# Kernel tuning notes

Measured on AMD Instinct MI355X. Metric: run time of the kernel, lower is better.

The kernel has to match this reference:

```python
import jax, jax.numpy as jnp
import numpy as np

C, CP, H, D, N, B = 128, 16, 8, 16, 2048, 1
INF = 1e8


def _ln(x, w=None, b=None, eps=1e-5):
    mu = jnp.mean(x, axis=-1, keepdims=True)
    var = jnp.var(x, axis=-1, keepdims=True)
    y = (x - mu) * jax.lax.rsqrt(var + eps)
    if w is not None:
        y = y * w
    if b is not None:
        y = y + b
    return y


def _ada_ln(a, s, sln_w, gw, gb, skw):
    # AdaLN: non-affine LN on a, weight-only LN on s, sigmoid gate + skip from s
    a = _ln(a)
    s = _ln(s, sln_w)
    return jax.nn.sigmoid(s @ gw + gb) * a + s @ skw


def _betas(n, n_keys=128, inf=INF):
    # centers at 16 + 32k; query row i belongs to window i//32, keys within +/- n_keys//2 of center
    i = jnp.arange(n)
    c = 16 + 32 * (i // 32)
    j = jnp.arange(n)
    ok = (j[None, :] >= (c - n_keys // 2)[:, None]) & (j[None, :] < (c + n_keys // 2)[:, None])
    return jnp.where(ok, 0.0, -inf).astype(jnp.float32)


def _forward(atom_single, atom_proj, atom_pair, mask,
             a_sln_w, a_gate_w, a_gate_b, a_skip_w,
             wq, bq, wk, wv, wg, bg, wo, bo,
             lnz_w, lnz_b, wz, wog, bog,
             t_sln_w, t_gate_w, t_gate_b, t_skip_w,
             w_sw, w_hid, w_out, t_wog, t_bog):
    bs, n, _ = atom_single.shape
    betas = _betas(n)
    # ---- AttentionPairBias (input_gating=True, residual handled outside) ----
    a = _ada_ln(atom_single, atom_proj, a_sln_w, a_gate_w, a_gate_b, a_skip_w)
    q = (a @ wq + bq).reshape(bs, n, H, D)
    k = (a @ wk).reshape(bs, n, H, D)
    v = (a @ wv).reshape(bs, n, H, D)
    pair_bias = _ln(atom_pair, lnz_w, lnz_b) @ wz            # (bs, n, n, H)
    pair_bias = jnp.transpose(pair_bias, (0, 3, 1, 2)) + betas  # (bs, H, n, n)
    mask_bias = (INF * (mask - 1.0))[:, None, None, :]          # (bs, 1, 1, n)
    logits = jnp.einsum('bqhd,bkhd->bhqk', q, k) / np.float32(np.sqrt(D))
    logits = logits + pair_bias + mask_bias
    probs = jax.nn.softmax(logits, axis=-1)
    o = jnp.einsum('bhqk,bkhd->bqhd', probs, v)
    g = jax.nn.sigmoid(a @ wg + bg).reshape(bs, n, H, D)
    o = (o * g).reshape(bs, n, H * D) @ wo + bo
    o = jax.nn.sigmoid(atom_proj @ wog + bog) * o             # conditioned output gate
    atom_single = atom_single + o
    # ---- ConditionedTransitionBlock (SwiGLU, n=2) ----
    t = _ada_ln(atom_single, atom_proj, t_sln_w, t_gate_w, t_gate_b, t_skip_w)
    hidden = jax.nn.silu(t @ w_sw) * (t @ w_hid)              # (bs, n, 2C)
    t_out = jax.nn.sigmoid(atom_proj @ t_wog + t_bog) * (hidden @ w_out)
    return atom_single + t_out


def setup_inputs() -> dict:
    key = jax.random.key(0)
    ks = iter(jax.random.split(key, 40))
    rn = lambda shape, s=1.0: jax.random.normal(next(ks), shape, jnp.float32) * s
    p = 0.05
    return {
        "atom_single": rn((B, N, C)),
        "atom_proj": rn((B, N, C)),
        "atom_pair": rn((B, N, N, CP)),
        "mask": jnp.ones((B, N), jnp.float32),
        "a_sln_w": jnp.ones((C,), jnp.float32), "a_gate_w": rn((C, C), p), "a_gate_b": jnp.zeros((C,), jnp.float32), "a_skip_w": rn((C, C), p),
        "wq": rn((C, C), p), "bq": jnp.zeros((C,), jnp.float32),
        "wk": rn((C, C), p), "wv": rn((C, C), p),
        "wg": rn((C, C), p), "bg": jnp.ones((C,), jnp.float32),
        "wo": rn((C, C), p), "bo": jnp.zeros((C,), jnp.float32),
        "lnz_w": jnp.ones((CP,), jnp.float32), "lnz_b": jnp.zeros((CP,), jnp.float32), "wz": rn((CP, H), p),
        "wog": rn((C, C), p), "bog": jnp.full((C,), -2.0, jnp.float32),
        "t_sln_w": jnp.ones((C,), jnp.float32), "t_gate_w": rn((C, C), p), "t_gate_b": jnp.zeros((C,), jnp.float32), "t_skip_w": rn((C, C), p),
        "w_sw": rn((C, 2 * C), p), "w_hid": rn((C, 2 * C), p), "w_out": rn((2 * C, C), p),
        "t_wog": rn((C, C), p), "t_bog": jnp.full((C,), -2.0, jnp.float32),
    }


def reference(atom_single, atom_proj, atom_pair, mask,
              a_sln_w, a_gate_w, a_gate_b, a_skip_w,
              wq, bq, wk, wv, wg, bg, wo, bo,
              lnz_w, lnz_b, wz, wog, bog,
              t_sln_w, t_gate_w, t_gate_b, t_skip_w,
              w_sw, w_hid, w_out, t_wog, t_bog):
    out = _forward(atom_single, atom_proj, atom_pair, mask,
                   a_sln_w, a_gate_w, a_gate_b, a_skip_w,
                   wq, bq, wk, wv, wg, bg, wo, bo,
                   lnz_w, lnz_b, wz, wog, bog,
                   t_sln_w, t_gate_w, t_gate_b, t_skip_w,
                   w_sw, w_hid, w_out, t_wog, t_bog)
    return (out, atom_proj, atom_pair)
```

## Files before the change

### kernel.cpp

```cpp
#include <hip/hip_runtime.h>
#include <math.h>

#define NN 2048
#define CC 128
#define HH 8
#define DD 16
#define NKEY 128
#define INFV 1e8f
#define NPR ((long)NN * CC / 4)
#define NCPTOT (NPR + (long)NN * NN * 4)
#define SLOT 2176
#define ANP 36
#define ASLOT 1152

__device__ __forceinline__ float sigm(float x) { return 1.f / (1.f + expf(-x)); }

struct Args {
  const float *atom_single, *atom_proj, *atom_pair, *mask;
  const float *a_sln_w, *a_gate_w, *a_gate_b, *a_skip_w;
  const float *wq, *bq, *wk, *wv, *wg, *bg, *wo, *bo;
  const float *lnz_w, *lnz_b, *wz, *wog, *bog;
  const float *t_sln_w, *t_gate_w, *t_gate_b, *t_skip_w;
  const float *w_sw, *w_hid, *w_out, *t_wog, *t_bog;
  float *out;
  float *s_ln_t, *a_mat, *qm, *km, *vm, *gm, *ogm, *single2, *t_mat, *hidden, *bias;
  long cut[8];
};

__device__ __forceinline__ void copy_span(const Args& a, int s, long rb, long nb, int tid) {
  long c0 = a.cut[s], c1 = a.cut[s + 1];
  const float4* proj4 = (const float4*)a.atom_proj;
  const float4* pair4 = (const float4*)a.atom_pair;
  float4* dst = (float4*)(a.out + (long)NN * CC);
  long stride = nb * 256;
  long i = c0 + rb * 256 + tid;
  for (; i + 3 * stride < c1; i += 4 * stride) {
    long i1 = i + stride, i2 = i + 2 * stride, i3 = i + 3 * stride;
    float4 x0 = (i  < NPR) ? proj4[i]  : pair4[i  - NPR];
    float4 x1 = (i1 < NPR) ? proj4[i1] : pair4[i1 - NPR];
    float4 x2 = (i2 < NPR) ? proj4[i2] : pair4[i2 - NPR];
    float4 x3 = (i3 < NPR) ? proj4[i3] : pair4[i3 - NPR];
    dst[i] = x0; dst[i1] = x1; dst[i2] = x2; dst[i3] = x3;
  }
  for (; i < c1; i += stride) dst[i] = (i < NPR) ? proj4[i] : pair4[i - NPR];
}

__device__ __forceinline__ void gsingle_pf(float* sm, int tid,
    const float* __restrict__ A1, const float* __restrict__ B1, int lda1, int ldb1, int K1,
    int r0, int c0, float acc1[4][4]) {
  float* buf0 = sm;
  float* buf1 = sm + 2 * SLOT;
  int tr = (tid >> 4) * 4, tc = (tid & 15) * 4;
  int ar = tid >> 5, ak = tid & 31;
  int bk = tid >> 6, bc = tid & 63;
  float pA[2][8], pB[2][8];
  auto LD = [&](int kb, int s) {
#pragma unroll
    for (int j = 0; j < 8; ++j) {
      pA[s][j] = A1[(long)(r0 + ar + 8 * j) * lda1 + kb + ak];
      pB[s][j] = B1[(long)(kb + bk + 4 * j) * ldb1 + c0 + bc];
    }
  };
  auto WR = [&](float* buf, int s) {
    float* B1s_ = buf + SLOT;
#pragma unroll
    for (int j = 0; j < 8; ++j) {
      buf[ak * 68 + ar + 8 * j] = pA[s][j];
      B1s_[(bk + 4 * j) * 68 + bc] = pB[s][j];
    }
  };
  auto CMP = [&](float* cur) {
    float* As_ = cur;
    float* B1s_ = cur + SLOT;
#pragma unroll 4
    for (int k = 0; k < 32; ++k) {
      float4 a1 = *(const float4*)&As_[k * 68 + tr];
      float4 b1 = *(const float4*)&B1s_[k * 68 + tc];
      float a1v[4] = {a1.x, a1.y, a1.z, a1.w};
      float b1v[4] = {b1.x, b1.y, b1.z, b1.w};
#pragma unroll
      for (int i = 0; i < 4; ++i)
#pragma unroll
        for (int j = 0; j < 4; ++j) acc1[i][j] = fmaf(a1v[i], b1v[j], acc1[i][j]);
    }
  };
  int nk = K1 / 32;
  LD(0, 0);
  if (nk > 1) LD(32, 1);
  WR(buf0, 0);
  __syncthreads();
  for (int kt = 0; kt < nk; kt += 2) {
    if (kt + 2 < nk) LD((kt + 2) * 32, 0);
    if (kt + 1 < nk) WR(buf1, 1);
    CMP(buf0);
    __syncthreads();
    if (kt + 1 >= nk) break;
    if (kt + 3 < nk) LD((kt + 3) * 32, 1);
    if (kt + 2 < nk) WR(buf0, 0);
    CMP(buf1);
    __syncthreads();
  }
}

template <bool SHA>
__device__ __forceinline__ void gdual32(float* sm, int tid,
    const float* __restrict__ A1, const float* __restrict__ B1, int lda1, int ldb1, int K1,
    const float* __restrict__ A2, const float* __restrict__ B2, int lda2, int ldb2, int K2,
    int r0, int c0, float acc1[2][4], float acc2[2][4]) {
  const int offB1 = ASLOT;
  const int offA2 = ASLOT + SLOT;
  const int offB2 = SHA ? (ASLOT + SLOT) : (2 * ASLOT + SLOT);
  const int bufsz = SHA ? (ASLOT + 2 * SLOT) : (2 * ASLOT + 2 * SLOT);
  float* buf0 = sm;
  float* buf1 = sm + bufsz;
  int tr2 = (tid >> 4) * 2, tc4 = (tid & 15) * 4;
  int ar = tid & 31, ak4 = (tid >> 5) * 4;
  int bk = tid >> 6, bc = tid & 63;
  float4 vA1[2], vA2[2];
  float pB1[2][8], pB2[2][8];

  auto LD = [&](int kb, int s, bool twof) {
    vA1[s] = *(const float4*)&A1[(long)(r0 + ar) * lda1 + kb + ak4];
#pragma unroll
    for (int j = 0; j < 8; ++j)
      pB1[s][j] = B1[(long)(kb + bk + 4 * j) * ldb1 + c0 + bc];
    if (twof) {
      if constexpr (!SHA) vA2[s] = *(const float4*)&A2[(long)(r0 + ar) * lda2 + kb + ak4];
#pragma unroll
      for (int j = 0; j < 8; ++j)
        pB2[s][j] = B2[(long)(kb + bk + 4 * j) * ldb2 + c0 + bc];
    }
  };
  auto WR = [&](float* buf, int s, bool twof) {
    float* As_ = buf;
    float* B1s_ = buf + offB1;
    As_[(ak4 + 0) * ANP + ar] = vA1[s].x;
    As_[(ak4 + 1) * ANP + ar] = vA1[s].y;
    As_[(ak4 + 2) * ANP + ar] = vA1[s].z;
    As_[(ak4 + 3) * ANP + ar] = vA1[s].w;
#pragma unroll
    for (int j = 0; j < 8; ++j) B1s_[(bk + 4 * j) * 68 + bc] = pB1[s][j];
    if (twof) {
      float* B2s_ = buf + offB2;
      if constexpr (!SHA) {
        float* A2s_ = buf + offA2;
        A2s_[(ak4 + 0) * ANP + ar] = vA2[s].x;
        A2s_[(ak4 + 1) * ANP + ar] = vA2[s].y;
        A2s_[(ak4 + 2) * ANP + ar] = vA2[s].z;
        A2s_[(ak4 + 3) * ANP + ar] = vA2[s].w;
      }
#pragma unroll
      for (int j = 0; j < 8; ++j) B2s_[(bk + 4 * j) * 68 + bc] = pB2[s][j];
    }
  };
  auto CMP = [&](float* cur, bool twoc) {
    float* As_ = cur;
    float* B1s_ = cur + offB1;
    float* A2s_ = cur + offA2;
    float* B2s_ = cur + offB2;
    if (twoc) {
#pragma unroll 4
      for (int k = 0; k < 32; ++k) {
        float2 a1 = *(const float2*)&As_[k * ANP + tr2];
        float4 b1 = *(const float4*)&B1s_[k * 68 + tc4];
        float4 b2 = *(const float4*)&B2s_[k * 68 + tc4];
        float2 a2;
        if constexpr (SHA) a2 = a1; else a2 = *(const float2*)&A2s_[k * ANP + tr2];
        float a1v[2] = {a1.x, a1.y};
        float a2v[2] = {a2.x, a2.y};
        float b1v[4] = {b1.x, b1.y, b1.z, b1.w};
        float b2v[4] = {b2.x, b2.y, b2.z, b2.w};
#pragma unroll
        for (int i = 0; i < 2; ++i)
#pragma unroll
          for (int j = 0; j < 4; ++j) {
            acc1[i][j] = fmaf(a1v[i], b1v[j], acc1[i][j]);
            acc2[i][j] = fmaf(a2v[i], b2v[j], acc2[i][j]);
          }
      }
    } else {
#pragma unroll 4
      for (int k = 0; k < 32; ++k) {
        float2 a1 = *(const float2*)&As_[k * ANP + tr2];
        float4 b1 = *(const float4*)&B1s_[k * 68 + tc4];
        float a1v[2] = {a1.x, a1.y};
        float b1v[4] = {b1.x, b1.y, b1.z, b1.w};
#pragma unroll
        for (int i = 0; i < 2; ++i)
#pragma unroll
          for (int j = 0; j < 4; ++j) acc1[i][j] = fmaf(a1v[i], b1v[j], acc1[i][j]);
      }
    }
  };

  int nk = K1 / 32;
  LD(0, 0, 0 < K2);
  if (nk > 1) LD(32, 1, 32 < K2);
  WR(buf0, 0, 0 < K2);
  __syncthreads();
  for (int kt = 0; kt < nk; kt += 2) {
    if (kt + 2 < nk) LD((kt + 2) * 32, 0, (kt + 2) * 32 < K2);
    if (kt + 1 < nk) WR(buf1, 1, (kt + 1) * 32 < K2);
    CMP(buf0, kt * 32 < K2);
    __syncthreads();
    if (kt + 1 >= nk) break;
    if (kt + 3 < nk) LD((kt + 3) * 32, 1, (kt + 3) * 32 < K2);
    if (kt + 2 < nk) WR(buf0, 0, (kt + 2) * 32 < K2);
    CMP(buf1, (kt + 1) * 32 < K2);
    __syncthreads();
  }
}

__device__ __forceinline__ void gdual32_ln(float* sm, int tid,
    const float* __restrict__ proj, const float* __restrict__ w_ln,
    const float* __restrict__ B1, const float* __restrict__ B2,
    int r0, int c0, const float* sst, float acc1[2][4], float acc2[2][4]) {
  const int offB1 = ASLOT;
  const int offB2 = ASLOT + SLOT;
  const int bufsz = ASLOT + 2 * SLOT;
  float* buf0 = sm;
  float* buf1 = sm + bufsz;
  int tr2 = (tid >> 4) * 2, tc4 = (tid & 15) * 4;
  int ar = tid & 31, ak4 = (tid >> 5) * 4;
  int bk = tid >> 6, bc = tid & 63;
  float4 vA1[2];
  float pB1[2][8], pB2[2][8];

  auto LD = [&](int kb, int s) {
    float4 raw = *(const float4*)&proj[(long)(r0 + ar) * CC + kb + ak4];
    float4 wv = *(const float4*)&w_ln[kb + ak4];
    float mu = sst[2 * ar], rs = sst[2 * ar + 1];
    vA1[s].x = (raw.x - mu) * rs * wv.x;
    vA1[s].y = (raw.y - mu) * rs * wv.y;
    vA1[s].z = (raw.z - mu) * rs * wv.z;
    vA1[s].w = (raw.w - mu) * rs * wv.w;
#pragma unroll
    for (int j = 0; j < 8; ++j) {
      pB1[s][j] = B1[(long)(kb + bk + 4 * j) * CC + c0 + bc];
      pB2[s][j] = B2[(long)(kb + bk + 4 * j) * CC + c0 + bc];
    }
  };
  auto WR = [&](float* buf, int s) {
    float* B1s_ = buf + offB1;
    float* B2s_ = buf + offB2;
    buf[(ak4 + 0) * ANP + ar] = vA1[s].x;
    buf[(ak4 + 1) * ANP + ar] = vA1[s].y;
    buf[(ak4 + 2) * ANP + ar] = vA1[s].z;
    buf[(ak4 + 3) * ANP + ar] = vA1[s].w;
#pragma unroll
    for (int j = 0; j < 8; ++j) {
      B1s_[(bk + 4 * j) * 68 + bc] = pB1[s][j];
      B2s_[(bk + 4 * j) * 68 + bc] = pB2[s][j];
    }
  };
  auto CMP = [&](float* cur) {
    float* As_ = cur;
    float* B1s_ = cur + offB1;
    float* B2s_ = cur + offB2;
#pragma unroll 4
    for (int k = 0; k < 32; ++k) {
      float2 a1 = *(const float2*)&As_[k * ANP + tr2];
      float4 b1 = *(const float4*)&B1s_[k * 68 + tc4];
      float4 b2 = *(const float4*)&B2s_[k * 68 + tc4];
      float a1v[2] = {a1.x, a1.y};
      float b1v[4] = {b1.x, b1.y, b1.z, b1.w};
      float b2v[4] = {b2.x, b2.y, b2.z, b2.w};
#pragma unroll
      for (int i = 0; i < 2; ++i)
#pragma unroll
        for (int j = 0; j < 4; ++j) {
          acc1[i][j] = fmaf(a1v[i], b1v[j], acc1[i][j]);
          acc2[i][j] = fmaf(a1v[i], b2v[j], acc2[i][j]);
        }
    }
  };

  LD(0, 0);
  LD(32, 1);
  WR(buf0, 0);
  __syncthreads();
  LD(64, 0);
  WR(buf1, 1);
  CMP(buf0);
  __syncthreads();
  LD(96, 1);
  WR(buf0, 0);
  CMP(buf1);
  __syncthreads();
  WR(buf1, 1);
  CMP(buf0);
  __syncthreads();
  CMP(buf1);
  __syncthreads();
}

__device__ __forceinline__ void bias_stage(const Args& a, long lo, long hi,
                                           int bid, int nb, int tid, float* sm) {
  float* swz = sm;
  float* swn = sm + 128;
  float* sbn = sm + 144;
  if (tid < 128) swz[tid] = a.wz[tid];
  else if (tid < 144) swn[tid - 128] = a.lnz_w[tid - 128];
  else if (tid < 160) sbn[tid - 144] = a.lnz_b[tid - 144];
  __syncthreads();
  for (long e = lo + bid * 256 + tid; e < hi; e += (long)nb * 256) {
    int q = (int)(e >> 7), kk = (int)(e & 127);
    int k = (q >> 5) * 32 - 48 + kk;
    float o[HH];
    if (k >= 0 && k < NN) {
      const float4* p = (const float4*)(a.atom_pair + ((long)q * NN + k) * 16);
      float4 x0 = p[0], x1 = p[1], x2 = p[2], x3 = p[3];
      float x[16] = {x0.x, x0.y, x0.z, x0.w, x1.x, x1.y, x1.z, x1.w,
                     x2.x, x2.y, x2.z, x2.w, x3.x, x3.y, x3.z, x3.w};
      float s = 0.f, ss = 0.f;
#pragma unroll
      for (int c = 0; c < 16; ++c) { s += x[c]; ss += x[c] * x[c]; }
      float mu = s * (1.f / 16.f);
      float r = rsqrtf(ss * (1.f / 16.f) - mu * mu + 1e-5f);
#pragma unroll
      for (int h = 0; h < HH; ++h) o[h] = 0.f;
#pragma unroll
      for (int c = 0; c < 16; ++c) {
        float y = (x[c] - mu) * r * swn[c] + sbn[c];
#pragma unroll
        for (int h = 0; h < HH; ++h) o[h] = fmaf(y, swz[c * HH + h], o[h]);
      }
      float mb = INFV * (a.mask[k] - 1.f);
#pragma unroll
      for (int h = 0; h < HH; ++h) o[h] += mb;
    } else {
#pragma unroll
      for (int h = 0; h < HH; ++h) o[h] = -INFV;
    }
#pragma unroll
    for (int h = 0; h < HH; ++h) a.bias[(long)h * NN * NKEY + e] = o[h];
  }
}

__device__ __forceinline__ void adaln_a_ln(const Args& a, int bid, int tid,
                                           float* sm, float* sst) {
  int r0 = (bid & 63) * 32, c0 = (bid >> 6) * 64;
  {
    int row = tid >> 3, cg = (tid & 7) * 16;
    const float* sp = a.atom_proj + (long)(r0 + row) * CC + cg;
    const float* ss_ = a.atom_single + (long)(r0 + row) * CC + cg;
    float s1 = 0.f, q1 = 0.f, s2 = 0.f, q2 = 0.f;
#pragma unroll
    for (int j = 0; j < 4; ++j) {
      float4 v = *(const float4*)(sp + j * 4);
      s1 += v.x + v.y + v.z + v.w;
      q1 += v.x * v.x + v.y * v.y + v.z * v.z + v.w * v.w;
      float4 u = *(const float4*)(ss_ + j * 4);
      s2 += u.x + u.y + u.z + u.w;
      q2 += u.x * u.x + u.y * u.y + u.z * u.z + u.w * u.w;
    }
#pragma unroll
    for (int m = 1; m < 8; m <<= 1) {
      s1 += __shfl_xor(s1, m); q1 += __shfl_xor(q1, m);
      s2 += __shfl_xor(s2, m); q2 += __shfl_xor(q2, m);
    }
    if ((tid & 7) == 0) {
      float mu1 = s1 * (1.f / CC);
      sst[2 * row] = mu1;
      sst[2 * row + 1] = rsqrtf(q1 * (1.f / CC) - mu1 * mu1 + 1e-5f);
      float mu2 = s2 * (1.f / CC);
      sst[64 + 2 * row] = mu2;
      sst[64 + 2 * row + 1] = rsqrtf(q2 * (1.f / CC) - mu2 * mu2 + 1e-5f);
    }
  }
  __syncthreads();
  float acc1[2][4] = {{0}}, acc2[2][4] = {{0}};
  gdual32_ln(sm, tid, a.atom_proj, a.a_sln_w, a.a_gate_w, a.a_skip_w,
             r0, c0, sst, acc1, acc2);
  int tr2 = (tid >> 4) * 2, tc4 = (tid & 15) * 4;
#pragma unroll
  for (int i = 0; i < 2; ++i) {
    long r = r0 + tr2 + i;
    float mup = sst[2 * (tr2 + i)], rsp = sst[2 * (tr2 + i) + 1];
    float mus = sst[64 + 2 * (tr2 + i)], rss = sst[64 + 2 * (tr2 + i) + 1];
    float4 sv = *(const float4*)(a.atom_single + r * CC + c0 + tc4);
    float4 pv = *(const float4*)(a.atom_proj + r * CC + c0 + tc4);
    float4 wt = *(const float4*)(a.t_sln_w + c0 + tc4);
    float lnm[4] = {(sv.x - mus) * rss, (sv.y - mus) * rss,
                    (sv.z - mus) * rss, (sv.w - mus) * rss};
    float lnp[4] = {(pv.x - mup) * rsp, (pv.y - mup) * rsp,
                    (pv.z - mup) * rsp, (pv.w - mup) * rsp};
    float wtv[4] = {wt.x, wt.y, wt.z, wt.w};
    float o[4];
#pragma unroll
    for (int j = 0; j < 4; ++j)
      o[j] = sigm(acc1[i][j] + a.a_gate_b[c0 + tc4 + j]) * lnm[j] + acc2[i][j];
    *(float4*)(a.a_mat + r * CC + c0 + tc4) = make_float4(o[0], o[1], o[2], o[3]);
    *(float4*)(a.s_ln_t + r * CC + c0 + tc4) =
        make_float4(lnp[0] * wtv[0], lnp[1] * wtv[1], lnp[2] * wtv[2], lnp[3] * wtv[3]);
  }
}

template <bool INLN>
__device__ __forceinline__ void adaln32_stage(const Args& a, const float* A, const float* gw,
                                              const float* gb, const float* skw,
                                              const float* lnm_or_src, float* outp,
                                              int bid, int tid, float* sm, float* sst) {
  int r0 = (bid & 63) * 32, c0 = (bid >> 6) * 64;
  if constexpr (INLN) {
    int row = tid >> 3, cg = (tid & 7) * 16;
    const float* src = lnm_or_src + (long)(r0 + row) * CC + cg;
    float s = 0.f, ss = 0.f;
#pragma unroll
    for (int j = 0; j < 4; ++j) {
      float4 v = *(const float4*)(src + j * 4);
      s += v.x + v.y + v.z + v.w;
      ss += v.x * v.x + v.y * v.y + v.z * v.z + v.w * v.w;
    }
#pragma unroll
    for (int m = 1; m < 8; m <<= 1) { s += __shfl_xor(s, m); ss += __shfl_xor(ss, m); }
    if ((tid & 7) == 0) {
      float mu = s * (1.f / CC);
      sst[2 * row] = mu;
      sst[2 * row + 1] = rsqrtf(ss * (1.f / CC) - mu * mu + 1e-5f);
    }
  }
  float acc1[2][4] = {{0}}, acc2[2][4] = {{0}};
  gdual32<true>(sm, tid, A, gw, 128, 128, 128, A, skw, 128, 128, 128, r0, c0, acc1, acc2);
  int tr2 = (tid >> 4) * 2, tc4 = (tid & 15) * 4;
#pragma unroll
  for (int i = 0; i < 2; ++i) {
    long r = r0 + tr2 + i;
    float lv[4];
    if constexpr (INLN) {
      float mu = sst[2 * (tr2 + i)], rr = sst[2 * (tr2 + i) + 1];
      float4 sv = *(const float4*)(lnm_or_src + r * CC + c0 + tc4);
      lv[0] = (sv.x - mu) * rr; lv[1] = (sv.y - mu) * rr;
      lv[2] = (sv.z - mu) * rr; lv[3] = (sv.w - mu) * rr;
    } else {
      float4 lm = *(const float4*)(lnm_or_src + r * CC + c0 + tc4);
      lv[0] = lm.x; lv[1] = lm.y; lv[2] = lm.z; lv[3] = lm.w;
    }
    float o[4];
#pragma unroll
    for (int j = 0; j < 4; ++j)
      o[j] = sigm(acc1[i][j] + gb[c0 + tc4 + j]) * lv[j] + acc2[i][j];
    *(float4*)(outp + r * CC + c0 + tc4) = make_float4(o[0], o[1], o[2], o[3]);
  }
}

__device__ __forceinline__ void gemm4_stage(const Args& a, int bid, int tid, float* sm) {
  int r0 = (bid & 31) * 64;
  int cg4 = (bid >> 5) * 64;
  int mat = cg4 >> 7;
  int c0 = cg4 & 127;
  const float* B = (mat == 0) ? a.wq : (mat == 1) ? a.wk : (mat == 2) ? a.wv : a.wg;
  float acc[4][4] = {{0}};
  gsingle_pf(sm, tid, a.a_mat, B, 128, 128, 128, r0, c0, acc);
  float* outp = (mat == 0) ? a.qm : (mat == 1) ? a.km : (mat == 2) ? a.vm : a.gm;
  int tr = (tid >> 4) * 4, tc = (tid & 15) * 4;
#pragma unroll
  for (int i = 0; i < 4; ++i) {
    long r = r0 + tr + i;
    float o[4];
#pragma unroll
    for (int j = 0; j < 4; ++j) {
      float x = acc[i][j];
      if (mat == 0) x += a.bq[c0 + tc + j];
      if (mat == 3) x = sigm(x + a.bg[c0 + tc + j]);
      o[j] = x;
    }
    *(float4*)(outp + r * CC + c0 + tc) = make_float4(o[0], o[1], o[2], o[3]);
  }
}

__device__ __forceinline__ void attn_unit(const Args& a, int u, int tid, float* sm) {
  int w = u & 63, h = u >> 6;
  int q0 = w * 32, k0 = w * 32 - 48;
  float* Qs = sm;
  float* Ks = sm + 544;
  float* Vs = sm + 3104;
  float* Ps = sm + 5664;
  for (int i = tid; i < 32 * 16; i += 256) {
    int qi = i >> 4, d = i & 15;
    Qs[qi * 17 + d] = a.qm[(long)(q0 + qi) * CC + h * DD + d];
  }
  for (int i = tid; i < 128 * 16; i += 256) {
    int kk = i >> 4, d = i & 15;
    int k = k0 + kk;
    bool ok = (k >= 0 && k < NN);
    Ks[kk * 20 + d] = ok ? a.km[(long)k * CC + h * DD + d] : 0.f;
    Vs[kk * 20 + d] = ok ? a.vm[(long)k * CC + h * DD + d] : 0.f;
  }
  __syncthreads();
  int qi = tid >> 3, kg = tid & 7;
  const float* brow = a.bias + (long)h * NN * NKEY + (long)(q0 + qi) * NKEY;
  float qreg[16];
#pragma unroll
  for (int d = 0; d < 16; ++d) qreg[d] = Qs[qi * 17 + d];
  float l[16];
#pragma unroll
  for (int j = 0; j < 16; ++j) {
    int kk = kg + 8 * j;
    const float4* kr = (const float4*)&Ks[kk * 20];
    float4 k0v = kr[0], k1v = kr[1], k2v = kr[2], k3v = kr[3];
    float acc = 0.f;
    acc = fmaf(qreg[0], k0v.x, acc);  acc = fmaf(qreg[1], k0v.y, acc);
    acc = fmaf(qreg[2], k0v.z, acc);  acc = fmaf(qreg[3], k0v.w, acc);
    acc = fmaf(qreg[4], k1v.x, acc);  acc = fmaf(qreg[5], k1v.y, acc);
    acc = fmaf(qreg[6], k1v.z, acc);  acc = fmaf(qreg[7], k1v.w, acc);
    acc = fmaf(qreg[8], k2v.x, acc);  acc = fmaf(qreg[9], k2v.y, acc);
    acc = fmaf(qreg[10], k2v.z, acc); acc = fmaf(qreg[11], k2v.w, acc);
    acc = fmaf(qreg[12], k3v.x, acc); acc = fmaf(qreg[13], k3v.y, acc);
    acc = fmaf(qreg[14], k3v.z, acc); acc = fmaf(qreg[15], k3v.w, acc);
    l[j] = acc * 0.25f + brow[kk];
  }
  float m = l[0];
#pragma unroll
  for (int j = 1; j < 16; ++j) m = fmaxf(m, l[j]);
#pragma unroll
  for (int mm = 1; mm < 8; mm <<= 1) m = fmaxf(m, __shfl_xor(m, mm));
  float sum = 0.f;
#pragma unroll
  for (int j = 0; j < 16; ++j) { l[j] = expf(l[j] - m); sum += l[j]; }
#pragma unroll
  for (int mm = 1; mm < 8; mm <<= 1) sum += __shfl_xor(sum, mm);
  float inv = 1.f / sum;
#pragma unroll
  for (int j = 0; j < 16; ++j) Ps[qi * 132 + kg + 8 * j] = l[j] * inv;
  __syncthreads();
  int d0 = tid & 7;
  float o0 = 0.f, o1 = 0.f;
#pragma unroll 8
  for (int kk = 0; kk < 128; ++kk) {
    float p = Ps[qi * 132 + kk];
    o0 = fmaf(p, Vs[kk * 20 + d0], o0);
    o1 = fmaf(p, Vs[kk * 20 + d0 + 8], o1);
  }
  long base = (long)(q0 + qi) * CC + h * DD;
  a.ogm[base + d0] = o0 * a.gm[base + d0];
  a.ogm[base + d0 + 8] = o1 * a.gm[base + d0 + 8];
}

__device__ __forceinline__ void out1_32(const Args& a, int bid, int tid, float* sm) {
  int r0 = (bid & 63) * 32, c0 = (bid >> 6) * 64;
  float accX[2][4] = {{0}}, accW[2][4] = {{0}};
  gdual32<false>(sm, tid, a.ogm, a.wo, 128, 128, 128, a.atom_proj, a.wog, 128, 128, 128,
                 r0, c0, accX, accW);
  int tr2 = (tid >> 4) * 2, tc4 = (tid & 15) * 4;
#pragma unroll
  for (int i = 0; i < 2; ++i) {
    long r = r0 + tr2 + i;
    float4 sv = *(const float4*)(a.atom_single + r * CC + c0 + tc4);
    float s[4] = {sv.x, sv.y, sv.z, sv.w};
    float o[4];
#pragma unroll
    for (int j = 0; j < 4; ++j) {
      int c = c0 + tc4 + j;
      o[j] = s[j] + sigm(accW[i][j] + a.bog[c]) * (accX[i][j] + a.bo[c]);
    }
    *(float4*)(a.single2 + r * CC + c0 + tc4) = make_float4(o[0], o[1], o[2], o[3]);
  }
}

__device__ __forceinline__ void swiglu_32(const Args& a, int bid, int tid, float* sm) {
  int r0 = (bid & 63) * 32, c0 = (bid >> 6) * 64;
  float acc1[2][4] = {{0}}, acc2[2][4] = {{0}};
  gdual32<true>(sm, tid, a.t_mat, a.w_sw, 128, 256, 128, a.t_mat, a.w_hid, 128, 256, 128,
                r0, c0, acc1, acc2);
  int tr2 = (tid >> 4) * 2, tc4 = (tid & 15) * 4;
#pragma unroll
  for (int i = 0; i < 2; ++i) {
    long r = r0 + tr2 + i;
    float o[4];
#pragma unroll
    for (int j = 0; j < 4; ++j) {
      float x = acc1[i][j];
      o[j] = x * sigm(x) * acc2[i][j];
    }
    *(float4*)(a.hidden + r * 256 + c0 + tc4) = make_float4(o[0], o[1], o[2], o[3]);
  }
}

__device__ __forceinline__ void out2_32(const Args& a, int bid, int tid, float* sm) {
  int r0 = (bid & 63) * 32, c0 = (bid >> 6) * 64;
  float accX[2][4] = {{0}}, accW[2][4] = {{0}};
  gdual32<false>(sm, tid, a.hidden, a.w_out, 256, 128, 256, a.atom_proj, a.t_wog, 128, 128, 128,
                 r0, c0, accX, accW);
  int tr2 = (tid >> 4) * 2, tc4 = (tid & 15) * 4;
#pragma unroll
  for (int i = 0; i < 2; ++i) {
    long r = r0 + tr2 + i;
    float4 sv = *(const float4*)(a.single2 + r * CC + c0 + tc4);
    float s[4] = {sv.x, sv.y, sv.z, sv.w};
    float o[4];
#pragma unroll
    for (int j = 0; j < 4; ++j) {
      int c = c0 + tc4 + j;
      o[j] = s[j] + sigm(accW[i][j] + a.t_bog[c]) * accX[i][j];
    }
    *(float4*)(a.out + r * CC + c0 + tc4) = make_float4(o[0], o[1], o[2], o[3]);
  }
}

#define BIAS_TOT ((long)NN * NKEY)
#define BIAS_H (BIAS_TOT / 2)

__global__ __launch_bounds__(256) void k_adaln_a(Args a) {
  __shared__ __align__(16) float sm[2 * (ASLOT + 2 * SLOT) + 128];
  int bid = blockIdx.x, tid = threadIdx.x;
  if (bid < 128) adaln_a_ln(a, bid, tid, sm, sm + 2 * (ASLOT + 2 * SLOT));
  else if (bid < 256) bias_stage(a, 0, BIAS_H, bid - 128, 128, tid, sm);
  else copy_span(a, 0, bid - 256, gridDim.x - 256, tid);
}

__global__ __launch_bounds__(256) void k_qkvg(Args a) {
  __shared__ __align__(16) float sm[2 * 2 * SLOT];
  int bid = blockIdx.x, tid = threadIdx.x;
  if (bid < 256) gemm4_stage(a, bid, tid, sm);
  else if (bid < 384) bias_stage(a, BIAS_H, BIAS_TOT, bid - 256, 128, tid, sm);
  else copy_span(a, 1, bid - 384, gridDim.x - 384, tid);
}

__global__ __launch_bounds__(256) void k_attn(Args a) {
  __shared__ __align__(16) float sm[9888];
  int bid = blockIdx.x, tid = threadIdx.x;
  if (bid < 512) attn_unit(a, bid, tid, sm);
  else copy_span(a, 2, bid - 512, gridDim.x - 512, tid);
}

__global__ __launch_bounds__(256) void k_out1(Args a) {
  __shared__ __align__(16) float sm[2 * (2 * ASLOT + 2 * SLOT)];
  int bid = blockIdx.x, tid = threadIdx.x;
  if (bid < 128) out1_32(a, bid, tid, sm);
  else copy_span(a, 3, bid - 128, gridDim.x - 128, tid);
}

__global__ __launch_bounds__(256) void k_adaln_t(Args a) {
  __shared__ __align__(16) float sm[2 * (ASLOT + 2 * SLOT) + 64];
  int bid = blockIdx.x, tid = threadIdx.x;
  if (bid < 128)
    adaln32_stage<true>(a, a.s_ln_t, a.t_gate_w, a.t_gate_b, a.t_skip_w, a.single2, a.t_mat,
                        bid, tid, sm, sm + 2 * (ASLOT + 2 * SLOT));
  else copy_span(a, 4, bid - 128, gridDim.x - 128, tid);
}

__global__ __launch_bounds__(256) void k_swiglu(Args a) {
  __shared__ __align__(16) float sm[2 * (ASLOT + 2 * SLOT)];
  int bid = blockIdx.x, tid = threadIdx.x;
  if (bid < 256) swiglu_32(a, bid, tid, sm);
  else copy_span(a, 5, bid - 256, gridDim.x - 256, tid);
}

__global__ __launch_bounds__(256) void k_out2(Args a) {
  __shared__ __align__(16) float sm[2 * (2 * ASLOT + 2 * SLOT)];
  int bid = blockIdx.x, tid = threadIdx.x;
  if (bid < 128) out2_32(a, bid, tid, sm);
  else copy_span(a, 6, bid - 128, gridDim.x - 128, tid);
}

extern "C" void kernel_launch(void* const* d_in, const int* in_sizes, int n_in,
                              void* d_out, int out_size, void* d_ws, size_t ws_size,
                              hipStream_t stream) {
  (void)in_sizes; (void)n_in; (void)out_size; (void)ws_size;
  Args a;
  a.atom_single = (const float*)d_in[0];
  a.atom_proj   = (const float*)d_in[1];
  a.atom_pair   = (const float*)d_in[2];
  a.mask        = (const float*)d_in[3];
  a.a_sln_w  = (const float*)d_in[4];
  a.a_gate_w = (const float*)d_in[5];
  a.a_gate_b = (const float*)d_in[6];
  a.a_skip_w = (const float*)d_in[7];
  a.wq = (const float*)d_in[8];  a.bq = (const float*)d_in[9];
  a.wk = (const float*)d_in[10]; a.wv = (const float*)d_in[11];
  a.wg = (const float*)d_in[12]; a.bg = (const float*)d_in[13];
  a.wo = (const float*)d_in[14]; a.bo = (const float*)d_in[15];
  a.lnz_w = (const float*)d_in[16]; a.lnz_b = (const float*)d_in[17];
  a.wz = (const float*)d_in[18];
  a.wog = (const float*)d_in[19]; a.bog = (const float*)d_in[20];
  a.t_sln_w  = (const float*)d_in[21];
  a.t_gate_w = (const float*)d_in[22];
  a.t_gate_b = (const float*)d_in[23];
  a.t_skip_w = (const float*)d_in[24];
  a.w_sw  = (const float*)d_in[25];
  a.w_hid = (const float*)d_in[26];
  a.w_out = (const float*)d_in[27];
  a.t_wog = (const float*)d_in[28];
  a.t_bog = (const float*)d_in[29];
  a.out = (float*)d_out;

  float* ws = (float*)d_ws;
  const long NC = (long)NN * CC;
  a.s_ln_t  = ws + 0 * NC;
  a.a_mat   = ws + 1 * NC;
  a.qm      = ws + 2 * NC;
  a.km      = ws + 3 * NC;
  a.vm      = ws + 4 * NC;
  a.gm      = ws + 5 * NC;
  a.ogm     = ws + 6 * NC;
  a.single2 = ws + 7 * NC;
  a.t_mat   = ws + 8 * NC;
  a.hidden  = ws + 9 * NC;
  a.bias    = ws + 11 * NC;

  const int cum[8] = {0, 11, 23, 37, 44, 51, 58, 64};
  for (int i = 0; i < 8; ++i) a.cut[i] = NCPTOT * (long)cum[i] / 64;

  k_adaln_a<<<2048, 256, 0, stream>>>(a);
  k_qkvg   <<<2048, 256, 0, stream>>>(a);
  k_attn   <<<2048, 256, 0, stream>>>(a);
  k_out1   <<<2048, 256, 0, stream>>>(a);
  k_adaln_t<<<2048, 256, 0, stream>>>(a);
  k_swiglu <<<2048, 256, 0, stream>>>(a);
  k_out2   <<<2048, 256, 0, stream>>>(a);
}
```

Before: 145.3 us.

## Fuse output projection and transition AdaLN into one kernel per row block

Merges the out1 stage and the transition AdaLN stage into a single kernel. Each block owns 32 full rows, computes both column halves of the attention output projection, derives the LayerNorm statistics from registers, then runs the gate/skip GEMMs. This removes one kernel launch and the re-read of single2 for the LN statistics. The cost is fewer compute blocks (64 instead of 128), each doing twice the sequential work, and the copy spans are rebalanced across the remaining kernels.

```diff
diff --git a/kernel.cpp b/kernel.cpp
--- a/kernel.cpp
+++ b/kernel.cpp
@@ -24,7 +24,7 @@
   const float *w_sw, *w_hid, *w_out, *t_wog, *t_bog;
   float *out;
   float *s_ln_t, *a_mat, *qm, *km, *vm, *gm, *ogm, *single2, *t_mat, *hidden, *bias;
-  long cut[8];
+  long cut[7];
 };
 
 __device__ __forceinline__ void copy_span(const Args& a, int s, long rb, long nb, int tid) {
@@ -396,54 +396,6 @@
   }
 }
 
-template <bool INLN>
-__device__ __forceinline__ void adaln32_stage(const Args& a, const float* A, const float* gw,
-                                              const float* gb, const float* skw,
-                                              const float* lnm_or_src, float* outp,
-                                              int bid, int tid, float* sm, float* sst) {
-  int r0 = (bid & 63) * 32, c0 = (bid >> 6) * 64;
-  if constexpr (INLN) {
-    int row = tid >> 3, cg = (tid & 7) * 16;
-    const float* src = lnm_or_src + (long)(r0 + row) * CC + cg;
-    float s = 0.f, ss = 0.f;
-#pragma unroll
-    for (int j = 0; j < 4; ++j) {
-      float4 v = *(const float4*)(src + j * 4);
-      s += v.x + v.y + v.z + v.w;
-      ss += v.x * v.x + v.y * v.y + v.z * v.z + v.w * v.w;
-    }
-#pragma unroll
-    for (int m = 1; m < 8; m <<= 1) { s += __shfl_xor(s, m); ss += __shfl_xor(ss, m); }
-    if ((tid & 7) == 0) {
-      float mu = s * (1.f / CC);
-      sst[2 * row] = mu;
-      sst[2 * row + 1] = rsqrtf(ss * (1.f / CC) - mu * mu + 1e-5f);
-    }
-  }
-  float acc1[2][4] = {{0}}, acc2[2][4] = {{0}};
-  gdual32<true>(sm, tid, A, gw, 128, 128, 128, A, skw, 128, 128, 128, r0, c0, acc1, acc2);
-  int tr2 = (tid >> 4) * 2, tc4 = (tid & 15) * 4;
-#pragma unroll
-  for (int i = 0; i < 2; ++i) {
-    long r = r0 + tr2 + i;
-    float lv[4];
-    if constexpr (INLN) {
-      float mu = sst[2 * (tr2 + i)], rr = sst[2 * (tr2 + i) + 1];
-      float4 sv = *(const float4*)(lnm_or_src + r * CC + c0 + tc4);
-      lv[0] = (sv.x - mu) * rr; lv[1] = (sv.y - mu) * rr;
-      lv[2] = (sv.z - mu) * rr; lv[3] = (sv.w - mu) * rr;
-    } else {
-      float4 lm = *(const float4*)(lnm_or_src + r * CC + c0 + tc4);
-      lv[0] = lm.x; lv[1] = lm.y; lv[2] = lm.z; lv[3] = lm.w;
-    }
-    float o[4];
-#pragma unroll
-    for (int j = 0; j < 4; ++j)
-      o[j] = sigm(acc1[i][j] + gb[c0 + tc4 + j]) * lv[j] + acc2[i][j];
-    *(float4*)(outp + r * CC + c0 + tc4) = make_float4(o[0], o[1], o[2], o[3]);
-  }
-}
-
 __device__ __forceinline__ void gemm4_stage(const Args& a, int bid, int tid, float* sm) {
   int r0 = (bid & 31) * 64;
   int cg4 = (bid >> 5) * 64;
@@ -537,24 +489,94 @@
   a.ogm[base + d0 + 8] = o1 * a.gm[base + d0 + 8];
 }
 
-__device__ __forceinline__ void out1_32(const Args& a, int bid, int tid, float* sm) {
-  int r0 = (bid & 63) * 32, c0 = (bid >> 6) * 64;
-  float accX[2][4] = {{0}}, accW[2][4] = {{0}};
-  gdual32<false>(sm, tid, a.ogm, a.wo, 128, 128, 128, a.atom_proj, a.wog, 128, 128, 128,
-                 r0, c0, accX, accW);
+__device__ __forceinline__ void back_merge(const Args& a, int bid, int tid, float* sm) {
+  int r0 = bid * 32;
   int tr2 = (tid >> 4) * 2, tc4 = (tid & 15) * 4;
+  float s2a[2][4], s2b[2][4];
+
+  {
+    float accX[2][4] = {{0}}, accW[2][4] = {{0}};
+    gdual32<false>(sm, tid, a.ogm, a.wo, 128, 128, 128, a.atom_proj, a.wog, 128, 128, 128,
+                   r0, 0, accX, accW);
+#pragma unroll
+    for (int i = 0; i < 2; ++i) {
+      long r = r0 + tr2 + i;
+      float4 sv = *(const float4*)(a.atom_single + r * CC + tc4);
+#pragma unroll
+      for (int j = 0; j < 4; ++j) {
+        int c = tc4 + j;
+        float sj = (j == 0) ? sv.x : (j == 1) ? sv.y : (j == 2) ? sv.z : sv.w;
+        s2a[i][j] = sj + sigm(accW[i][j] + a.bog[c]) * (accX[i][j] + a.bo[c]);
+      }
+      *(float4*)(a.single2 + r * CC + tc4) =
+          make_float4(s2a[i][0], s2a[i][1], s2a[i][2], s2a[i][3]);
+    }
+  }
+  {
+    float accX[2][4] = {{0}}, accW[2][4] = {{0}};
+    gdual32<false>(sm, tid, a.ogm, a.wo, 128, 128, 128, a.atom_proj, a.wog, 128, 128, 128,
+                   r0, 64, accX, accW);
+#pragma unroll
+    for (int i = 0; i < 2; ++i) {
+      long r = r0 + tr2 + i;
+      float4 sv = *(const float4*)(a.atom_single + r * CC + 64 + tc4);
+#pragma unroll
+      for (int j = 0; j < 4; ++j) {
+        int c = 64 + tc4 + j;
+        float sj = (j == 0) ? sv.x : (j == 1) ? sv.y : (j == 2) ? sv.z : sv.w;
+        s2b[i][j] = sj + sigm(accW[i][j] + a.bog[c]) * (accX[i][j] + a.bo[c]);
+      }
+      *(float4*)(a.single2 + r * CC + 64 + tc4) =
+          make_float4(s2b[i][0], s2b[i][1], s2b[i][2], s2b[i][3]);
+    }
+  }
+
+  float mu[2], rs[2];
 #pragma unroll
   for (int i = 0; i < 2; ++i) {
-    long r = r0 + tr2 + i;
-    float4 sv = *(const float4*)(a.atom_single + r * CC + c0 + tc4);
-    float s[4] = {sv.x, sv.y, sv.z, sv.w};
-    float o[4];
-#pragma unroll
-    for (int j = 0; j < 4; ++j) {
-      int c = c0 + tc4 + j;
-      o[j] = s[j] + sigm(accW[i][j] + a.bog[c]) * (accX[i][j] + a.bo[c]);
-    }
-    *(float4*)(a.single2 + r * CC + c0 + tc4) = make_float4(o[0], o[1], o[2], o[3]);
+    float s = s2a[i][0] + s2a[i][1] + s2a[i][2] + s2a[i][3]
+            + s2b[i][0] + s2b[i][1] + s2b[i][2] + s2b[i][3];
+    float q = s2a[i][0] * s2a[i][0] + s2a[i][1] * s2a[i][1]
+            + s2a[i][2] * s2a[i][2] + s2a[i][3] * s2a[i][3]
+            + s2b[i][0] * s2b[i][0] + s2b[i][1] * s2b[i][1]
+            + s2b[i][2] * s2b[i][2] + s2b[i][3] * s2b[i][3];
+#pragma unroll
+    for (int m = 1; m < 16; m <<= 1) { s += __shfl_xor(s, m); q += __shfl_xor(q, m); }
+    mu[i] = s * (1.f / CC);
+    rs[i] = rsqrtf(q * (1.f / CC) - mu[i] * mu[i] + 1e-5f);
+  }
+
+  {
+    float ac1[2][4] = {{0}}, ac2[2][4] = {{0}};
+    gdual32<true>(sm, tid, a.s_ln_t, a.t_gate_w, 128, 128, 128,
+                  a.s_ln_t, a.t_skip_w, 128, 128, 128, r0, 0, ac1, ac2);
+#pragma unroll
+    for (int i = 0; i < 2; ++i) {
+      long r = r0 + tr2 + i;
+      float o[4];
+#pragma unroll
+      for (int j = 0; j < 4; ++j) {
+        float lv = (s2a[i][j] - mu[i]) * rs[i];
+        o[j] = sigm(ac1[i][j] + a.t_gate_b[tc4 + j]) * lv + ac2[i][j];
+      }
+      *(float4*)(a.t_mat + r * CC + tc4) = make_float4(o[0], o[1], o[2], o[3]);
+    }
+  }
+  {
+    float ac1[2][4] = {{0}}, ac2[2][4] = {{0}};
+    gdual32<true>(sm, tid, a.s_ln_t, a.t_gate_w, 128, 128, 128,
+                  a.s_ln_t, a.t_skip_w, 128, 128, 128, r0, 64, ac1, ac2);
+#pragma unroll
+    for (int i = 0; i < 2; ++i) {
+      long r = r0 + tr2 + i;
+      float o[4];
+#pragma unroll
+      for (int j = 0; j < 4; ++j) {
+        float lv = (s2b[i][j] - mu[i]) * rs[i];
+        o[j] = sigm(ac1[i][j] + a.t_gate_b[64 + tc4 + j]) * lv + ac2[i][j];
+      }
+      *(float4*)(a.t_mat + r * CC + 64 + tc4) = make_float4(o[0], o[1], o[2], o[3]);
+    }
   }
 }
 
@@ -624,34 +646,25 @@
   else copy_span(a, 2, bid - 512, gridDim.x - 512, tid);
 }
 
-__global__ __launch_bounds__(256) void k_out1(Args a) {
+__global__ __launch_bounds__(256) void k_back(Args a) {
   __shared__ __align__(16) float sm[2 * (2 * ASLOT + 2 * SLOT)];
   int bid = blockIdx.x, tid = threadIdx.x;
-  if (bid < 128) out1_32(a, bid, tid, sm);
-  else copy_span(a, 3, bid - 128, gridDim.x - 128, tid);
-}
-
-__global__ __launch_bounds__(256) void k_adaln_t(Args a) {
-  __shared__ __align__(16) float sm[2 * (ASLOT + 2 * SLOT) + 64];
-  int bid = blockIdx.x, tid = threadIdx.x;
-  if (bid < 128)
-    adaln32_stage<true>(a, a.s_ln_t, a.t_gate_w, a.t_gate_b, a.t_skip_w, a.single2, a.t_mat,
-                        bid, tid, sm, sm + 2 * (ASLOT + 2 * SLOT));
-  else copy_span(a, 4, bid - 128, gridDim.x - 128, tid);
+  if (bid < 64) back_merge(a, bid, tid, sm);
+  else copy_span(a, 3, bid - 64, gridDim.x - 64, tid);
 }
 
 __global__ __launch_bounds__(256) void k_swiglu(Args a) {
   __shared__ __align__(16) float sm[2 * (ASLOT + 2 * SLOT)];
   int bid = blockIdx.x, tid = threadIdx.x;
   if (bid < 256) swiglu_32(a, bid, tid, sm);
-  else copy_span(a, 5, bid - 256, gridDim.x - 256, tid);
+  else copy_span(a, 4, bid - 256, gridDim.x - 256, tid);
 }
 
 __global__ __launch_bounds__(256) void k_out2(Args a) {
   __shared__ __align__(16) float sm[2 * (2 * ASLOT + 2 * SLOT)];
   int bid = blockIdx.x, tid = threadIdx.x;
   if (bid < 128) out2_32(a, bid, tid, sm);
-  else copy_span(a, 6, bid - 128, gridDim.x - 128, tid);
+  else copy_span(a, 5, bid - 128, gridDim.x - 128, tid);
 }
 
 extern "C" void kernel_launch(void* const* d_in, const int* in_sizes, int n_in,
@@ -699,14 +712,13 @@
   a.hidden  = ws + 9 * NC;
   a.bias    = ws + 11 * NC;
 
-  const int cum[8] = {0, 11, 23, 37, 44, 51, 58, 64};
-  for (int i = 0; i < 8; ++i) a.cut[i] = NCPTOT * (long)cum[i] / 64;
+  const int cum[7] = {0, 11, 23, 38, 47, 56, 64};
+  for (int i = 0; i < 7; ++i) a.cut[i] = NCPTOT * (long)cum[i] / 64;
 
   k_adaln_a<<<2048, 256, 0, stream>>>(a);
   k_qkvg   <<<2048, 256, 0, stream>>>(a);
   k_attn   <<<2048, 256, 0, stream>>>(a);
-  k_out1   <<<2048, 256, 0, stream>>>(a);
-  k_adaln_t<<<2048, 256, 0, stream>>>(a);
+  k_back   <<<2048, 256, 0, stream>>>(a);
   k_swiglu <<<2048, 256, 0, stream>>>(a);
   k_out2   <<<2048, 256, 0, stream>>>(a);
 }
```

Measured after the change: 161.3 us. 11.0% more time.
